# Optimization experiments

Measured on AMD Instinct MI355X. Metric: run time of the kernel, lower is better.

Reference implementation:

```python
import jax, jax.numpy as jnp
import numpy as np

WIN = (4, 4, 4)   # (wd, wh, ww), window seq len s = 64
HEADS = 4


def setup_inputs() -> dict:
    key = jax.random.key(0)
    k1, k2, k3 = jax.random.split(key, 3)
    B, D, H, W, C = 1, 32, 64, 128, 96
    x = jax.random.normal(k1, (B, D, H, W, C), dtype=jnp.float32)
    # weights stored in (in, out) layout; math identical to torch Linear (x @ W.T)
    w_qkv = jax.random.normal(k2, (C, 3 * C), dtype=jnp.float32) * (C ** -0.5)
    w_proj = jax.random.normal(k3, (C, C), dtype=jnp.float32) * (C ** -0.5)
    b_proj = jnp.zeros((C,), dtype=jnp.float32)
    return {"x": x, "w_qkv": w_qkv, "w_proj": w_proj, "b_proj": b_proj}


def reference(x, w_qkv, w_proj, b_proj):
    B, D, H, W, C = x.shape
    wd, wh, ww = WIN
    h = HEADS
    ch = C // h
    s = wd * wh * ww
    scale = ch ** -0.5
    n, m, l = D // wd, H // wh, W // ww
    # window partition: [B,D,H,W,C] -> [B,n,m,l,s,C]
    xw = x.reshape(B, n, wd, m, wh, l, ww, C)
    xw = xw.transpose(0, 1, 3, 5, 2, 4, 6, 7).reshape(B, n, m, l, s, C)
    # QKV projection (no bias)
    qkv = xw @ w_qkv                      # [B,n,m,l,s,3C]
    q, k, v = jnp.split(qkv, 3, axis=-1)  # each [B,n,m,l,s,C]

    def to_heads(t):
        return t.reshape(B, n, m, l, s, h, ch).transpose(0, 1, 2, 3, 5, 4, 6)

    q, k, v = to_heads(q), to_heads(k), to_heads(v)  # [B,n,m,l,h,s,ch]
    attn = jnp.einsum('bnmlhsc,bnmlhtc->bnmlhst', q, k) * scale
    attn = jax.nn.softmax(attn, axis=-1)             # [B,n,m,l,h,s,s]
    out = jnp.einsum('bnmlhst,bnmlhtc->bnmlhsc', attn, v)
    # merge heads: [B,n,m,l,h,s,ch] -> [B,n,m,l,s,C]
    out = out.transpose(0, 1, 2, 3, 5, 4, 6).reshape(B, n, m, l, s, C)
    out = out @ w_proj + b_proj
    # window merge back to [B,D,H,W,C]
    out = out.reshape(B, n, m, l, wd, wh, ww, C)
    out = out.transpose(0, 1, 4, 2, 5, 3, 6, 7).reshape(B, D, H, W, C)
    return out
```

## Files before the change

kernel.cpp:

```cpp
#include <hip/hip_runtime.h>
#include <hip/hip_bf16.h>

typedef __attribute__((ext_vector_type(8))) short bf16x8;
typedef __attribute__((ext_vector_type(4))) float f32x4;
typedef __attribute__((ext_vector_type(4))) unsigned short u16x4;
typedef __attribute__((ext_vector_type(4))) unsigned int u32x4;
typedef __attribute__((ext_vector_type(2))) unsigned int u32x2;

#define MFMA16(a, b, c) __builtin_amdgcn_mfma_f32_16x16x32_bf16((a), (b), (c), 0, 0, 0)

#define WQT_ELEMS 27648
#define WPT_ELEMS 9216

__device__ __forceinline__ unsigned short cvt_bf(float f) {
    __hip_bfloat16 h = __float2bfloat16(f);
    return *reinterpret_cast<unsigned short*>(&h);
}
__device__ __forceinline__ unsigned pack2bf(float a, float b) {
    return (unsigned)cvt_bf(a) | ((unsigned)cvt_bf(b) << 16);
}

__global__ void wconv_kernel(const float* __restrict__ wqkv,
                             const float* __restrict__ wproj,
                             unsigned short* __restrict__ wsT) {
    int o = blockIdx.x * 256 + threadIdx.x;
    if (o < WQT_ELEMS) {
        int j = o / 96, c = o % 96;
        float w = wqkv[c * 288 + j];
        if (j < 96) w *= 0.2944889313f;
        wsT[o] = cvt_bf(w);
    } else if (o < WQT_ELEMS + WPT_ELEMS) {
        int o2 = o - WQT_ELEMS;
        int j = o2 / 96, c = o2 % 96;
        wsT[o] = cvt_bf(wproj[c * 96 + j]);
    }
}

__device__ __forceinline__ int xq_addr(int t, int c) {
    return ((c >> 5) << 12) + ((t >> 1) << 7)
         + ((((t & 1) << 6) + ((c & 31) << 1)) ^ (((t >> 1) & 7) << 4));
}

#define LOADW(m, W0, W1, W2) do {                                              \
    const unsigned short* _wp = wsT + ((m) * 16 + p) * 96 + qg * 8;            \
    W0 = *reinterpret_cast<const bf16x8*>(_wp);                                \
    W1 = *reinterpret_cast<const bf16x8*>(_wp + 32);                           \
    W2 = *reinterpret_cast<const bf16x8*>(_wp + 64);                           \
} while (0)

#define MFMA_T(W0, W1, W2)                                                     \
    f32x4 ac0 = fzero, ac1 = fzero, ac2 = fzero, ac3 = fzero;                  \
    __builtin_amdgcn_s_setprio(1);                                             \
    ac0 = MFMA16(W0, a00, ac0); ac1 = MFMA16(W0, a10, ac1);                    \
    ac2 = MFMA16(W0, a20, ac2); ac3 = MFMA16(W0, a30, ac3);                    \
    ac0 = MFMA16(W1, a01, ac0); ac1 = MFMA16(W1, a11, ac1);                    \
    ac2 = MFMA16(W1, a21, ac2); ac3 = MFMA16(W1, a31, ac3);                    \
    ac0 = MFMA16(W2, a02, ac0); ac1 = MFMA16(W2, a12, ac1);                    \
    ac2 = MFMA16(W2, a22, ac2); ac3 = MFMA16(W2, a32, ac3);                    \
    __builtin_amdgcn_s_setprio(0);

#define DO_QK(DST, ch, W0, W1, W2) do {                                        \
    MFMA_T(W0, W1, W2)                                                         \
    char* _d = (DST) + xq_addr(p, (ch));                                       \
    *reinterpret_cast<u32x2*>(_d)        = (u32x2){pack2bf(ac0[0],ac0[1]), pack2bf(ac0[2],ac0[3])}; \
    *reinterpret_cast<u32x2*>(_d + 1024) = (u32x2){pack2bf(ac1[0],ac1[1]), pack2bf(ac1[2],ac1[3])}; \
    *reinterpret_cast<u32x2*>(_d + 2048) = (u32x2){pack2bf(ac2[0],ac2[1]), pack2bf(ac2[2],ac2[3])}; \
    *reinterpret_cast<u32x2*>(_d + 3072) = (u32x2){pack2bf(ac3[0],ac3[1]), pack2bf(ac3[2],ac3[3])}; \
} while (0)

#define DO_Q(m, W0, W1, W2) DO_QK(xq, (m) * 16 + 4 * qg, W0, W1, W2)
#define DO_K(m, W0, W1, W2) DO_QK(kb, ((m) - 6) * 16 + 4 * qg, W0, W1, W2)

#define STV1(JV, A, T2) do {                                                   \
    int _r0 = (JV);                                                            \
    *reinterpret_cast<unsigned short*>(vtb + (_r0)     * 128 + ((T2) ^ (((_r0)     & 7) << 4))) = cvt_bf(A[0]); \
    *reinterpret_cast<unsigned short*>(vtb + (_r0 + 1) * 128 + ((T2) ^ (((_r0 + 1) & 7) << 4))) = cvt_bf(A[1]); \
    *reinterpret_cast<unsigned short*>(vtb + (_r0 + 2) * 128 + ((T2) ^ (((_r0 + 2) & 7) << 4))) = cvt_bf(A[2]); \
    *reinterpret_cast<unsigned short*>(vtb + (_r0 + 3) * 128 + ((T2) ^ (((_r0 + 3) & 7) << 4))) = cvt_bf(A[3]); \
} while (0)

#define DO_V(m, W0, W1, W2) do {                                               \
    MFMA_T(W0, W1, W2)                                                         \
    int jv = ((m) - 12) * 16 + 4 * qg;                                         \
    STV1(jv, ac0, (p) * 2);                                                    \
    STV1(jv, ac1, (16 + p) * 2);                                               \
    STV1(jv, ac2, (32 + p) * 2);                                               \
    STV1(jv, ac3, (48 + p) * 2);                                               \
} while (0)

#define LOADWP(m, W0, W1, W2) do {                                             \
    const unsigned short* _wp = wpT + ((m) * 16 + p) * 96 + qg * 8;            \
    W0 = *reinterpret_cast<const bf16x8*>(_wp);                                \
    W1 = *reinterpret_cast<const bf16x8*>(_wp + 32);                           \
    W2 = *reinterpret_cast<const bf16x8*>(_wp + 64);                           \
} while (0)

#define PROJ(m, W0, W1, W2) do {                                               \
    f32x4 acc = fzero;                                                         \
    __builtin_amdgcn_s_setprio(1);                                             \
    acc = MFMA16(W0, o0, acc);                                                 \
    acc = MFMA16(W1, o1, acc);                                                 \
    acc = MFMA16(W2, o2, acc);                                                 \
    __builtin_amdgcn_s_setprio(0);                                             \
    float4 bb = *reinterpret_cast<const float4*>(bproj + (m) * 16 + 4 * qg);   \
    f32x4 r;                                                                   \
    r[0] = acc[0] + bb.x; r[1] = acc[1] + bb.y;                                \
    r[2] = acc[2] + bb.z; r[3] = acc[3] + bb.w;                                \
    *reinterpret_cast<f32x4*>(out + obase + (m) * 16 + 4 * qg) = r;            \
} while (0)

__global__ __launch_bounds__(256) __attribute__((amdgpu_waves_per_eu(3, 4)))
void winattn_kernel(const float* __restrict__ x,
                    const unsigned short* __restrict__ wsT,
                    const float* __restrict__ bproj,
                    float* __restrict__ out) {
    __shared__ __align__(16) char LDS[37888];
    char* xq  = LDS;
    char* kb  = LDS + 12288;
    char* vtb = LDS + 24576;

    const int tid = threadIdx.x;
    const int lane = tid & 63;
    const int wv = tid >> 6;
    const int p  = lane & 15;
    const int qg = lane >> 4;

    const int iw  = blockIdx.x;
    const int l_i = iw & 31;
    const int m_i = (iw >> 5) & 15;
    const int n_i = iw >> 9;

    const f32x4 fzero = {0.f, 0.f, 0.f, 0.f};
    const bf16x8 zero8 = {0, 0, 0, 0, 0, 0, 0, 0};

    bf16x8 wA0, wA1, wA2, wB0, wB1, wB2;
    const int tb0 = (wv < 3) ? wv * 4 : 15;
    LOADW(tb0, wA0, wA1, wA2);

    {
        int t = tid / 24, cq = tid - t * 24;
        #pragma unroll
        for (int it = 0; it < 6; ++it) {
            int td = t >> 4, th = (t >> 2) & 3, tw = t & 3;
            int off = (((n_i * 4 + td) * 64 + (m_i * 4 + th)) * 128 + (l_i * 4 + tw)) * 96 + cq * 4;
            float4 v4 = *reinterpret_cast<const float4*>(x + off);
            u16x4 h;
            h[0] = cvt_bf(v4.x); h[1] = cvt_bf(v4.y); h[2] = cvt_bf(v4.z); h[3] = cvt_bf(v4.w);
            *reinterpret_cast<u16x4*>(xq + xq_addr(t, cq * 4)) = h;
            cq += 16;
            int carry = (cq >= 24) ? 1 : 0;
            cq -= carry ? 24 : 0;
            t += 10 + carry;
        }
    }
    __syncthreads();

    bf16x8 a00, a01, a02, a10, a11, a12, a20, a21, a22, a30, a31, a32;
    {
        const char* xb0 = xq + xq_addr(p, qg * 8);
        const char* xb1 = xq + xq_addr(p, 32 + qg * 8);
        const char* xb2 = xq + xq_addr(p, 64 + qg * 8);
        a00 = *reinterpret_cast<const bf16x8*>(xb0);
        a01 = *reinterpret_cast<const bf16x8*>(xb1);
        a02 = *reinterpret_cast<const bf16x8*>(xb2);
        a10 = *reinterpret_cast<const bf16x8*>(xb0 + 1024);
        a11 = *reinterpret_cast<const bf16x8*>(xb1 + 1024);
        a12 = *reinterpret_cast<const bf16x8*>(xb2 + 1024);
        a20 = *reinterpret_cast<const bf16x8*>(xb0 + 2048);
        a21 = *reinterpret_cast<const bf16x8*>(xb1 + 2048);
        a22 = *reinterpret_cast<const bf16x8*>(xb2 + 2048);
        a30 = *reinterpret_cast<const bf16x8*>(xb0 + 3072);
        a31 = *reinterpret_cast<const bf16x8*>(xb1 + 3072);
        a32 = *reinterpret_cast<const bf16x8*>(xb2 + 3072);
    }
    __syncthreads();

    if (wv == 0) {
        LOADW(1,  wB0, wB1, wB2); DO_Q(0,  wA0, wA1, wA2);
        LOADW(2,  wA0, wA1, wA2); DO_Q(1,  wB0, wB1, wB2);
        LOADW(3,  wB0, wB1, wB2); DO_Q(2,  wA0, wA1, wA2);
        LOADW(12, wA0, wA1, wA2); DO_Q(3,  wB0, wB1, wB2);
        DO_V(12, wA0, wA1, wA2);
    } else if (wv == 1) {
        LOADW(5,  wB0, wB1, wB2); DO_Q(4,  wA0, wA1, wA2);
        LOADW(6,  wA0, wA1, wA2); DO_Q(5,  wB0, wB1, wB2);
        LOADW(7,  wB0, wB1, wB2); DO_K(6,  wA0, wA1, wA2);
        LOADW(13, wA0, wA1, wA2); DO_K(7,  wB0, wB1, wB2);
        DO_V(13, wA0, wA1, wA2);
    } else if (wv == 2) {
        LOADW(9,  wB0, wB1, wB2); DO_K(8,  wA0, wA1, wA2);
        LOADW(10, wA0, wA1, wA2); DO_K(9,  wB0, wB1, wB2);
        LOADW(11, wB0, wB1, wB2); DO_K(10, wA0, wA1, wA2);
        LOADW(14, wA0, wA1, wA2); DO_K(11, wB0, wB1, wB2);
        DO_V(14, wA0, wA1, wA2);
    } else {
        LOADW(16, wB0, wB1, wB2); DO_V(15, wA0, wA1, wA2);
        LOADW(17, wA0, wA1, wA2); DO_V(16, wB0, wB1, wB2);
        DO_V(17, wA0, wA1, wA2);
    }
    __syncthreads();

    #pragma unroll 2
    for (int hd = 0; hd < 4; ++hd) {
        int qc = hd * 24 + qg * 8;
        bf16x8 aq_raw = *reinterpret_cast<const bf16x8*>(xq + xq_addr(wv * 16 + p, qc));
        bf16x8 aqh = (qg == 3) ? zero8 : aq_raw;
        const char* akb = kb + xq_addr(p, qc);
        f32x4 sacc[4];
        __builtin_amdgcn_s_setprio(1);
        sacc[0] = MFMA16(*reinterpret_cast<const bf16x8*>(akb),        aqh, fzero);
        sacc[1] = MFMA16(*reinterpret_cast<const bf16x8*>(akb + 1024), aqh, fzero);
        sacc[2] = MFMA16(*reinterpret_cast<const bf16x8*>(akb + 2048), aqh, fzero);
        sacc[3] = MFMA16(*reinterpret_cast<const bf16x8*>(akb + 3072), aqh, fzero);
        __builtin_amdgcn_s_setprio(0);
        float sum = 0.f;
        unsigned pk[4][2];
        #pragma unroll
        for (int nt = 0; nt < 4; ++nt) {
            float e0 = exp2f(sacc[nt][0]);
            float e1 = exp2f(sacc[nt][1]);
            float e2 = exp2f(sacc[nt][2]);
            float e3 = exp2f(sacc[nt][3]);
            sum += (e0 + e1) + (e2 + e3);
            pk[nt][0] = pack2bf(e0, e1);
            pk[nt][1] = pack2bf(e2, e3);
        }
        u32x4 pa0, pa1;
        #pragma unroll
        for (int d = 0; d < 4; ++d) {
            int src = ((qg & 1) * 2 + (d >> 1)) * 16 + p;
            int lo0 = __shfl((int)pk[0][d & 1], src);
            int hi0 = __shfl((int)pk[1][d & 1], src);
            int lo1 = __shfl((int)pk[2][d & 1], src);
            int hi1 = __shfl((int)pk[3][d & 1], src);
            pa0[d] = (qg < 2) ? (unsigned)lo0 : (unsigned)hi0;
            pa1[d] = (qg < 2) ? (unsigned)lo1 : (unsigned)hi1;
        }
        bf16x8 pA0 = __builtin_bit_cast(bf16x8, pa0);
        bf16x8 pA1 = __builtin_bit_cast(bf16x8, pa1);
        sum += __shfl_xor(sum, 16);
        sum += __shfl_xor(sum, 32);
        float inv = 1.0f / sum;
        f32x4 oacc[2] = {fzero, fzero};
        __builtin_amdgcn_s_setprio(1);
        #pragma unroll
        for (int n2 = 0; n2 < 2; ++n2) {
            int vr = hd * 24 + n2 * 16 + p;
            int rb = vr * 128, sw = (vr & 7) << 4;
            bf16x8 av0 = *reinterpret_cast<const bf16x8*>(vtb + rb + ((qg * 16) ^ sw));
            bf16x8 av1 = *reinterpret_cast<const bf16x8*>(vtb + rb + ((64 + qg * 16) ^ sw));
            oacc[n2] = MFMA16(av0, pA0, oacc[n2]);
            oacc[n2] = MFMA16(av1, pA1, oacc[n2]);
        }
        __builtin_amdgcn_s_setprio(0);
        {
            u32x2 w0 = { pack2bf(oacc[0][0] * inv, oacc[0][1] * inv),
                         pack2bf(oacc[0][2] * inv, oacc[0][3] * inv) };
            *reinterpret_cast<u32x2*>(xq + xq_addr(wv * 16 + p, hd * 24 + 4 * qg)) = w0;
            if (qg < 2) {
                u32x2 w1 = { pack2bf(oacc[1][0] * inv, oacc[1][1] * inv),
                             pack2bf(oacc[1][2] * inv, oacc[1][3] * inv) };
                *reinterpret_cast<u32x2*>(xq + xq_addr(wv * 16 + p, hd * 24 + 16 + 4 * qg)) = w1;
            }
        }
    }

    bf16x8 o0, o1, o2;
    o0 = *reinterpret_cast<const bf16x8*>(xq + xq_addr(wv * 16 + p, qg * 8));
    o1 = *reinterpret_cast<const bf16x8*>(xq + xq_addr(wv * 16 + p, 32 + qg * 8));
    o2 = *reinterpret_cast<const bf16x8*>(xq + xq_addr(wv * 16 + p, 64 + qg * 8));

    const int obase = (((n_i * 4 + wv) * 64 + (m_i * 4 + (p >> 2))) * 128
                       + (l_i * 4 + (p & 3))) * 96;
    const unsigned short* wpT = wsT + WQT_ELEMS;
    LOADWP(0, wA0, wA1, wA2);
    LOADWP(1, wB0, wB1, wB2); PROJ(0, wA0, wA1, wA2);
    LOADWP(2, wA0, wA1, wA2); PROJ(1, wB0, wB1, wB2);
    LOADWP(3, wB0, wB1, wB2); PROJ(2, wA0, wA1, wA2);
    LOADWP(4, wA0, wA1, wA2); PROJ(3, wB0, wB1, wB2);
    LOADWP(5, wB0, wB1, wB2); PROJ(4, wA0, wA1, wA2);
    PROJ(5, wB0, wB1, wB2);
}

extern "C" void kernel_launch(void* const* d_in, const int* in_sizes, int n_in,
                              void* d_out, int out_size, void* d_ws, size_t ws_size,
                              hipStream_t stream) {
    const float* x     = (const float*)d_in[0];
    const float* wqkv  = (const float*)d_in[1];
    const float* wproj = (const float*)d_in[2];
    const float* bproj = (const float*)d_in[3];
    float* out = (float*)d_out;
    unsigned short* wsT = (unsigned short*)d_ws;

    wconv_kernel<<<dim3((WQT_ELEMS + WPT_ELEMS) / 256), dim3(256), 0, stream>>>(wqkv, wproj, wsT);
    winattn_kernel<<<dim3(4096), dim3(256), 0, stream>>>(x, wsT, bproj, out);
}
```

Before: 72.59 us.

## Make window attention kernel persistent with double-buffered prefetch of next window

Launches 768 persistent blocks that loop over the 4096 windows, rather than one block per window. The next window's input is loaded from global memory into registers during the QKV projection and then stored into a second LDS buffer, and the two buffers swap each iteration. This is meant to hide global load latency and cut block launch overhead. In exchange, LDS per block grows to about 50KB, which may limit occupancy, and with 768 blocks over 4096 windows the work is unevenly split (some blocks do 6 windows, others 5).

```diff
diff --git a/kernel.cpp b/kernel.cpp
--- a/kernel.cpp
+++ b/kernel.cpp
@@ -11,6 +11,8 @@
 
 #define WQT_ELEMS 27648
 #define WPT_ELEMS 9216
+#define NWIN 4096
+#define NBLK 768
 
 __device__ __forceinline__ unsigned short cvt_bf(float f) {
     __hip_bfloat16 h = __float2bfloat16(f);
@@ -109,15 +111,30 @@
     *reinterpret_cast<f32x4*>(out + obase + (m) * 16 + 4 * qg) = r;            \
 } while (0)
 
-__global__ __launch_bounds__(256) __attribute__((amdgpu_waves_per_eu(3, 4)))
+#define STX(DST, LA, S) do {                                                   \
+    u16x4 _h;                                                                  \
+    _h[0] = cvt_bf(S[0]); _h[1] = cvt_bf(S[1]);                                \
+    _h[2] = cvt_bf(S[2]); _h[3] = cvt_bf(S[3]);                                \
+    *reinterpret_cast<u16x4*>((DST) + (LA)) = _h;                              \
+} while (0)
+
+#define MKO(K) do {                                                            \
+    int _td = t >> 4, _th = (t >> 2) & 3, _tw = t & 3;                         \
+    toff##K = ((_td * 64 + _th) * 128 + _tw) * 96 + cq * 4;                    \
+    lda##K  = xq_addr(t, cq * 4);                                              \
+    cq += 16; int _c = (cq >= 24) ? 1 : 0; cq -= _c ? 24 : 0; t += 10 + _c;    \
+} while (0)
+
+__global__ __launch_bounds__(256, 3)
 void winattn_kernel(const float* __restrict__ x,
                     const unsigned short* __restrict__ wsT,
                     const float* __restrict__ bproj,
                     float* __restrict__ out) {
-    __shared__ __align__(16) char LDS[37888];
-    char* xq  = LDS;
-    char* kb  = LDS + 12288;
-    char* vtb = LDS + 24576;
+    __shared__ __align__(16) char LDS[50176];
+    char* const kb  = LDS + 24576;
+    char* const vtb = LDS + 36864;
+    char* xq = LDS;
+    char* xn = LDS + 12288;
 
     const int tid = threadIdx.x;
     const int lane = tid & 63;
@@ -125,161 +142,182 @@
     const int p  = lane & 15;
     const int qg = lane >> 4;
 
-    const int iw  = blockIdx.x;
-    const int l_i = iw & 31;
-    const int m_i = (iw >> 5) & 15;
-    const int n_i = iw >> 9;
-
     const f32x4 fzero = {0.f, 0.f, 0.f, 0.f};
     const bf16x8 zero8 = {0, 0, 0, 0, 0, 0, 0, 0};
-
-    bf16x8 wA0, wA1, wA2, wB0, wB1, wB2;
     const int tb0 = (wv < 3) ? wv * 4 : 15;
-    LOADW(tb0, wA0, wA1, wA2);
-
+
+    int toff0, toff1, toff2, toff3, toff4, toff5;
+    int lda0, lda1, lda2, lda3, lda4, lda5;
     {
         int t = tid / 24, cq = tid - t * 24;
-        #pragma unroll
-        for (int it = 0; it < 6; ++it) {
-            int td = t >> 4, th = (t >> 2) & 3, tw = t & 3;
-            int off = (((n_i * 4 + td) * 64 + (m_i * 4 + th)) * 128 + (l_i * 4 + tw)) * 96 + cq * 4;
-            float4 v4 = *reinterpret_cast<const float4*>(x + off);
-            u16x4 h;
-            h[0] = cvt_bf(v4.x); h[1] = cvt_bf(v4.y); h[2] = cvt_bf(v4.z); h[3] = cvt_bf(v4.w);
-            *reinterpret_cast<u16x4*>(xq + xq_addr(t, cq * 4)) = h;
-            cq += 16;
-            int carry = (cq >= 24) ? 1 : 0;
-            cq -= carry ? 24 : 0;
-            t += 10 + carry;
-        }
+        MKO(0); MKO(1); MKO(2); MKO(3); MKO(4); MKO(5);
+    }
+
+    {
+        int iw = blockIdx.x;
+        const float* xb = x + 96 * ((iw >> 9) * 32768 + ((iw >> 5) & 15) * 512 + (iw & 31) * 4);
+        f32x4 v0 = *reinterpret_cast<const f32x4*>(xb + toff0);
+        f32x4 v1 = *reinterpret_cast<const f32x4*>(xb + toff1);
+        f32x4 v2 = *reinterpret_cast<const f32x4*>(xb + toff2);
+        f32x4 v3 = *reinterpret_cast<const f32x4*>(xb + toff3);
+        f32x4 v4 = *reinterpret_cast<const f32x4*>(xb + toff4);
+        f32x4 v5 = *reinterpret_cast<const f32x4*>(xb + toff5);
+        STX(xq, lda0, v0); STX(xq, lda1, v1); STX(xq, lda2, v2);
+        STX(xq, lda3, v3); STX(xq, lda4, v4); STX(xq, lda5, v5);
     }
     __syncthreads();
 
-    bf16x8 a00, a01, a02, a10, a11, a12, a20, a21, a22, a30, a31, a32;
-    {
-        const char* xb0 = xq + xq_addr(p, qg * 8);
-        const char* xb1 = xq + xq_addr(p, 32 + qg * 8);
-        const char* xb2 = xq + xq_addr(p, 64 + qg * 8);
-        a00 = *reinterpret_cast<const bf16x8*>(xb0);
-        a01 = *reinterpret_cast<const bf16x8*>(xb1);
-        a02 = *reinterpret_cast<const bf16x8*>(xb2);
-        a10 = *reinterpret_cast<const bf16x8*>(xb0 + 1024);
-        a11 = *reinterpret_cast<const bf16x8*>(xb1 + 1024);
-        a12 = *reinterpret_cast<const bf16x8*>(xb2 + 1024);
-        a20 = *reinterpret_cast<const bf16x8*>(xb0 + 2048);
-        a21 = *reinterpret_cast<const bf16x8*>(xb1 + 2048);
-        a22 = *reinterpret_cast<const bf16x8*>(xb2 + 2048);
-        a30 = *reinterpret_cast<const bf16x8*>(xb0 + 3072);
-        a31 = *reinterpret_cast<const bf16x8*>(xb1 + 3072);
-        a32 = *reinterpret_cast<const bf16x8*>(xb2 + 3072);
+    #pragma unroll 1
+    for (int iw = blockIdx.x; iw < NWIN; iw += NBLK) {
+        const int l_i = iw & 31;
+        const int m_i = (iw >> 5) & 15;
+        const int n_i = iw >> 9;
+
+        bf16x8 wA0, wA1, wA2, wB0, wB1, wB2;
+        LOADW(tb0, wA0, wA1, wA2);
+        bf16x8 a00, a01, a02, a10, a11, a12, a20, a21, a22, a30, a31, a32;
+        {
+            const char* xb0 = xq + xq_addr(p, qg * 8);
+            const char* xb1 = xq + xq_addr(p, 32 + qg * 8);
+            const char* xb2 = xq + xq_addr(p, 64 + qg * 8);
+            a00 = *reinterpret_cast<const bf16x8*>(xb0);
+            a01 = *reinterpret_cast<const bf16x8*>(xb1);
+            a02 = *reinterpret_cast<const bf16x8*>(xb2);
+            a10 = *reinterpret_cast<const bf16x8*>(xb0 + 1024);
+            a11 = *reinterpret_cast<const bf16x8*>(xb1 + 1024);
+            a12 = *reinterpret_cast<const bf16x8*>(xb2 + 1024);
+            a20 = *reinterpret_cast<const bf16x8*>(xb0 + 2048);
+            a21 = *reinterpret_cast<const bf16x8*>(xb1 + 2048);
+            a22 = *reinterpret_cast<const bf16x8*>(xb2 + 2048);
+            a30 = *reinterpret_cast<const bf16x8*>(xb0 + 3072);
+            a31 = *reinterpret_cast<const bf16x8*>(xb1 + 3072);
+            a32 = *reinterpret_cast<const bf16x8*>(xb2 + 3072);
+        }
+        __syncthreads();
+
+        const int iwn = iw + NBLK;
+        f32x4 s0, s1, s2, s3, s4, s5;
+        if (iwn < NWIN) {
+            const float* xb = x + 96 * ((iwn >> 9) * 32768 + ((iwn >> 5) & 15) * 512 + (iwn & 31) * 4);
+            s0 = *reinterpret_cast<const f32x4*>(xb + toff0);
+            s1 = *reinterpret_cast<const f32x4*>(xb + toff1);
+            s2 = *reinterpret_cast<const f32x4*>(xb + toff2);
+            s3 = *reinterpret_cast<const f32x4*>(xb + toff3);
+            s4 = *reinterpret_cast<const f32x4*>(xb + toff4);
+            s5 = *reinterpret_cast<const f32x4*>(xb + toff5);
+        }
+
+        if (wv == 0) {
+            LOADW(1,  wB0, wB1, wB2); DO_Q(0,  wA0, wA1, wA2);
+            LOADW(2,  wA0, wA1, wA2); DO_Q(1,  wB0, wB1, wB2);
+            LOADW(3,  wB0, wB1, wB2); DO_Q(2,  wA0, wA1, wA2);
+            LOADW(12, wA0, wA1, wA2); DO_Q(3,  wB0, wB1, wB2);
+            DO_V(12, wA0, wA1, wA2);
+        } else if (wv == 1) {
+            LOADW(5,  wB0, wB1, wB2); DO_Q(4,  wA0, wA1, wA2);
+            LOADW(6,  wA0, wA1, wA2); DO_Q(5,  wB0, wB1, wB2);
+            LOADW(7,  wB0, wB1, wB2); DO_K(6,  wA0, wA1, wA2);
+            LOADW(13, wA0, wA1, wA2); DO_K(7,  wB0, wB1, wB2);
+            DO_V(13, wA0, wA1, wA2);
+        } else if (wv == 2) {
+            LOADW(9,  wB0, wB1, wB2); DO_K(8,  wA0, wA1, wA2);
+            LOADW(10, wA0, wA1, wA2); DO_K(9,  wB0, wB1, wB2);
+            LOADW(11, wB0, wB1, wB2); DO_K(10, wA0, wA1, wA2);
+            LOADW(14, wA0, wA1, wA2); DO_K(11, wB0, wB1, wB2);
+            DO_V(14, wA0, wA1, wA2);
+        } else {
+            LOADW(16, wB0, wB1, wB2); DO_V(15, wA0, wA1, wA2);
+            LOADW(17, wA0, wA1, wA2); DO_V(16, wB0, wB1, wB2);
+            DO_V(17, wA0, wA1, wA2);
+        }
+        if (iwn < NWIN) {
+            STX(xn, lda0, s0); STX(xn, lda1, s1); STX(xn, lda2, s2);
+            STX(xn, lda3, s3); STX(xn, lda4, s4); STX(xn, lda5, s5);
+        }
+        __syncthreads();
+
+        #pragma unroll 2
+        for (int hd = 0; hd < 4; ++hd) {
+            int qc = hd * 24 + qg * 8;
+            bf16x8 aq_raw = *reinterpret_cast<const bf16x8*>(xq + xq_addr(wv * 16 + p, qc));
+            bf16x8 aqh = (qg == 3) ? zero8 : aq_raw;
+            const char* akb = kb + xq_addr(p, qc);
+            f32x4 sacc[4];
+            __builtin_amdgcn_s_setprio(1);
+            sacc[0] = MFMA16(*reinterpret_cast<const bf16x8*>(akb),        aqh, fzero);
+            sacc[1] = MFMA16(*reinterpret_cast<const bf16x8*>(akb + 1024), aqh, fzero);
+            sacc[2] = MFMA16(*reinterpret_cast<const bf16x8*>(akb + 2048), aqh, fzero);
+            sacc[3] = MFMA16(*reinterpret_cast<const bf16x8*>(akb + 3072), aqh, fzero);
+            __builtin_amdgcn_s_setprio(0);
+            float sum = 0.f;
+            unsigned pk[4][2];
+            #pragma unroll
+            for (int nt = 0; nt < 4; ++nt) {
+                float e0 = exp2f(sacc[nt][0]);
+                float e1 = exp2f(sacc[nt][1]);
+                float e2 = exp2f(sacc[nt][2]);
+                float e3 = exp2f(sacc[nt][3]);
+                sum += (e0 + e1) + (e2 + e3);
+                pk[nt][0] = pack2bf(e0, e1);
+                pk[nt][1] = pack2bf(e2, e3);
+            }
+            u32x4 pa0, pa1;
+            #pragma unroll
+            for (int d = 0; d < 4; ++d) {
+                int src = ((qg & 1) * 2 + (d >> 1)) * 16 + p;
+                int lo0 = __shfl((int)pk[0][d & 1], src);
+                int hi0 = __shfl((int)pk[1][d & 1], src);
+                int lo1 = __shfl((int)pk[2][d & 1], src);
+                int hi1 = __shfl((int)pk[3][d & 1], src);
+                pa0[d] = (qg < 2) ? (unsigned)lo0 : (unsigned)hi0;
+                pa1[d] = (qg < 2) ? (unsigned)lo1 : (unsigned)hi1;
+            }
+            bf16x8 pA0 = __builtin_bit_cast(bf16x8, pa0);
+            bf16x8 pA1 = __builtin_bit_cast(bf16x8, pa1);
+            sum += __shfl_xor(sum, 16);
+            sum += __shfl_xor(sum, 32);
+            float inv = 1.0f / sum;
+            f32x4 oacc[2] = {fzero, fzero};
+            __builtin_amdgcn_s_setprio(1);
+            #pragma unroll
+            for (int n2 = 0; n2 < 2; ++n2) {
+                int vr = hd * 24 + n2 * 16 + p;
+                int rb = vr * 128, sw = (vr & 7) << 4;
+                bf16x8 av0 = *reinterpret_cast<const bf16x8*>(vtb + rb + ((qg * 16) ^ sw));
+                bf16x8 av1 = *reinterpret_cast<const bf16x8*>(vtb + rb + ((64 + qg * 16) ^ sw));
+                oacc[n2] = MFMA16(av0, pA0, oacc[n2]);
+                oacc[n2] = MFMA16(av1, pA1, oacc[n2]);
+            }
+            __builtin_amdgcn_s_setprio(0);
+            {
+                u32x2 w0 = { pack2bf(oacc[0][0] * inv, oacc[0][1] * inv),
+                             pack2bf(oacc[0][2] * inv, oacc[0][3] * inv) };
+                *reinterpret_cast<u32x2*>(xq + xq_addr(wv * 16 + p, hd * 24 + 4 * qg)) = w0;
+                if (qg < 2) {
+                    u32x2 w1 = { pack2bf(oacc[1][0] * inv, oacc[1][1] * inv),
+                                 pack2bf(oacc[1][2] * inv, oacc[1][3] * inv) };
+                    *reinterpret_cast<u32x2*>(xq + xq_addr(wv * 16 + p, hd * 24 + 16 + 4 * qg)) = w1;
+                }
+            }
+        }
+
+        bf16x8 o0, o1, o2;
+        o0 = *reinterpret_cast<const bf16x8*>(xq + xq_addr(wv * 16 + p, qg * 8));
+        o1 = *reinterpret_cast<const bf16x8*>(xq + xq_addr(wv * 16 + p, 32 + qg * 8));
+        o2 = *reinterpret_cast<const bf16x8*>(xq + xq_addr(wv * 16 + p, 64 + qg * 8));
+        const int obase = (((n_i * 4 + wv) * 64 + (m_i * 4 + (p >> 2))) * 128
+                           + (l_i * 4 + (p & 3))) * 96;
+        const unsigned short* wpT = wsT + WQT_ELEMS;
+        LOADWP(0, wA0, wA1, wA2);
+        LOADWP(1, wB0, wB1, wB2); PROJ(0, wA0, wA1, wA2);
+        LOADWP(2, wA0, wA1, wA2); PROJ(1, wB0, wB1, wB2);
+        LOADWP(3, wB0, wB1, wB2); PROJ(2, wA0, wA1, wA2);
+        LOADWP(4, wA0, wA1, wA2); PROJ(3, wB0, wB1, wB2);
+        LOADWP(5, wB0, wB1, wB2); PROJ(4, wA0, wA1, wA2);
+        PROJ(5, wB0, wB1, wB2);
+
+        char* tp = xq; xq = xn; xn = tp;
     }
-    __syncthreads();
-
-    if (wv == 0) {
-        LOADW(1,  wB0, wB1, wB2); DO_Q(0,  wA0, wA1, wA2);
-        LOADW(2,  wA0, wA1, wA2); DO_Q(1,  wB0, wB1, wB2);
-        LOADW(3,  wB0, wB1, wB2); DO_Q(2,  wA0, wA1, wA2);
-        LOADW(12, wA0, wA1, wA2); DO_Q(3,  wB0, wB1, wB2);
-        DO_V(12, wA0, wA1, wA2);
-    } else if (wv == 1) {
-        LOADW(5,  wB0, wB1, wB2); DO_Q(4,  wA0, wA1, wA2);
-        LOADW(6,  wA0, wA1, wA2); DO_Q(5,  wB0, wB1, wB2);
-        LOADW(7,  wB0, wB1, wB2); DO_K(6,  wA0, wA1, wA2);
-        LOADW(13, wA0, wA1, wA2); DO_K(7,  wB0, wB1, wB2);
-        DO_V(13, wA0, wA1, wA2);
-    } else if (wv == 2) {
-        LOADW(9,  wB0, wB1, wB2); DO_K(8,  wA0, wA1, wA2);
-        LOADW(10, wA0, wA1, wA2); DO_K(9,  wB0, wB1, wB2);
-        LOADW(11, wB0, wB1, wB2); DO_K(10, wA0, wA1, wA2);
-        LOADW(14, wA0, wA1, wA2); DO_K(11, wB0, wB1, wB2);
-        DO_V(14, wA0, wA1, wA2);
-    } else {
-        LOADW(16, wB0, wB1, wB2); DO_V(15, wA0, wA1, wA2);
-        LOADW(17, wA0, wA1, wA2); DO_V(16, wB0, wB1, wB2);
-        DO_V(17, wA0, wA1, wA2);
-    }
-    __syncthreads();
-
-    #pragma unroll 2
-    for (int hd = 0; hd < 4; ++hd) {
-        int qc = hd * 24 + qg * 8;
-        bf16x8 aq_raw = *reinterpret_cast<const bf16x8*>(xq + xq_addr(wv * 16 + p, qc));
-        bf16x8 aqh = (qg == 3) ? zero8 : aq_raw;
-        const char* akb = kb + xq_addr(p, qc);
-        f32x4 sacc[4];
-        __builtin_amdgcn_s_setprio(1);
-        sacc[0] = MFMA16(*reinterpret_cast<const bf16x8*>(akb),        aqh, fzero);
-        sacc[1] = MFMA16(*reinterpret_cast<const bf16x8*>(akb + 1024), aqh, fzero);
-        sacc[2] = MFMA16(*reinterpret_cast<const bf16x8*>(akb + 2048), aqh, fzero);
-        sacc[3] = MFMA16(*reinterpret_cast<const bf16x8*>(akb + 3072), aqh, fzero);
-        __builtin_amdgcn_s_setprio(0);
-        float sum = 0.f;
-        unsigned pk[4][2];
-        #pragma unroll
-        for (int nt = 0; nt < 4; ++nt) {
-            float e0 = exp2f(sacc[nt][0]);
-            float e1 = exp2f(sacc[nt][1]);
-            float e2 = exp2f(sacc[nt][2]);
-            float e3 = exp2f(sacc[nt][3]);
-            sum += (e0 + e1) + (e2 + e3);
-            pk[nt][0] = pack2bf(e0, e1);
-            pk[nt][1] = pack2bf(e2, e3);
-        }
-        u32x4 pa0, pa1;
-        #pragma unroll
-        for (int d = 0; d < 4; ++d) {
-            int src = ((qg & 1) * 2 + (d >> 1)) * 16 + p;
-            int lo0 = __shfl((int)pk[0][d & 1], src);
-            int hi0 = __shfl((int)pk[1][d & 1], src);
-            int lo1 = __shfl((int)pk[2][d & 1], src);
-            int hi1 = __shfl((int)pk[3][d & 1], src);
-            pa0[d] = (qg < 2) ? (unsigned)lo0 : (unsigned)hi0;
-            pa1[d] = (qg < 2) ? (unsigned)lo1 : (unsigned)hi1;
-        }
-        bf16x8 pA0 = __builtin_bit_cast(bf16x8, pa0);
-        bf16x8 pA1 = __builtin_bit_cast(bf16x8, pa1);
-        sum += __shfl_xor(sum, 16);
-        sum += __shfl_xor(sum, 32);
-        float inv = 1.0f / sum;
-        f32x4 oacc[2] = {fzero, fzero};
-        __builtin_amdgcn_s_setprio(1);
-        #pragma unroll
-        for (int n2 = 0; n2 < 2; ++n2) {
-            int vr = hd * 24 + n2 * 16 + p;
-            int rb = vr * 128, sw = (vr & 7) << 4;
-            bf16x8 av0 = *reinterpret_cast<const bf16x8*>(vtb + rb + ((qg * 16) ^ sw));
-            bf16x8 av1 = *reinterpret_cast<const bf16x8*>(vtb + rb + ((64 + qg * 16) ^ sw));
-            oacc[n2] = MFMA16(av0, pA0, oacc[n2]);
-            oacc[n2] = MFMA16(av1, pA1, oacc[n2]);
-        }
-        __builtin_amdgcn_s_setprio(0);
-        {
-            u32x2 w0 = { pack2bf(oacc[0][0] * inv, oacc[0][1] * inv),
-                         pack2bf(oacc[0][2] * inv, oacc[0][3] * inv) };
-            *reinterpret_cast<u32x2*>(xq + xq_addr(wv * 16 + p, hd * 24 + 4 * qg)) = w0;
-            if (qg < 2) {
-                u32x2 w1 = { pack2bf(oacc[1][0] * inv, oacc[1][1] * inv),
-                             pack2bf(oacc[1][2] * inv, oacc[1][3] * inv) };
-                *reinterpret_cast<u32x2*>(xq + xq_addr(wv * 16 + p, hd * 24 + 16 + 4 * qg)) = w1;
-            }
-        }
-    }
-
-    bf16x8 o0, o1, o2;
-    o0 = *reinterpret_cast<const bf16x8*>(xq + xq_addr(wv * 16 + p, qg * 8));
-    o1 = *reinterpret_cast<const bf16x8*>(xq + xq_addr(wv * 16 + p, 32 + qg * 8));
-    o2 = *reinterpret_cast<const bf16x8*>(xq + xq_addr(wv * 16 + p, 64 + qg * 8));
-
-    const int obase = (((n_i * 4 + wv) * 64 + (m_i * 4 + (p >> 2))) * 128
-                       + (l_i * 4 + (p & 3))) * 96;
-    const unsigned short* wpT = wsT + WQT_ELEMS;
-    LOADWP(0, wA0, wA1, wA2);
-    LOADWP(1, wB0, wB1, wB2); PROJ(0, wA0, wA1, wA2);
-    LOADWP(2, wA0, wA1, wA2); PROJ(1, wB0, wB1, wB2);
-    LOADWP(3, wB0, wB1, wB2); PROJ(2, wA0, wA1, wA2);
-    LOADWP(4, wA0, wA1, wA2); PROJ(3, wB0, wB1, wB2);
-    LOADWP(5, wB0, wB1, wB2); PROJ(4, wA0, wA1, wA2);
-    PROJ(5, wB0, wB1, wB2);
 }
 
 extern "C" void kernel_launch(void* const* d_in, const int* in_sizes, int n_in,
@@ -293,5 +331,5 @@
     unsigned short* wsT = (unsigned short*)d_ws;
 
     wconv_kernel<<<dim3((WQT_ELEMS + WPT_ELEMS) / 256), dim3(256), 0, stream>>>(wqkv, wproj, wsT);
-    winattn_kernel<<<dim3(4096), dim3(256), 0, stream>>>(x, wsT, bproj, out);
-}
+    winattn_kernel<<<dim3(NBLK), dim3(256), 0, stream>>>(x, wsT, bproj, out);
+}
```

After: 212.4 us. 2.93x slower.
